# Kernel tuning notes

Measured on AMD Instinct MI355X. Metric: run time of the kernel, lower is better.

The kernel has to match this reference:

```python
import jax, jax.numpy as jnp
import numpy as np

N_NODES = 500000
D_FEAT = 128
BATCH = 16384
K_NEIGH = 32
N_MASKS = 4  # module hardcodes 4 masks with exponents 0.5*j (gcn path)


def setup_inputs() -> dict:
    key = jax.random.key(0)
    k1, k2, k3 = jax.random.split(key, 3)
    embed = jax.random.normal(k1, (N_NODES, D_FEAT), dtype=jnp.float32)
    neigh_idx = jax.random.randint(k2, (BATCH, K_NEIGH), 0, N_NODES, dtype=jnp.int32)
    # positive weights (original uses 1+degree counts; any positive weight is valid)
    neigh_w = jax.random.uniform(k3, (BATCH, K_NEIGH), dtype=jnp.float32, minval=0.05, maxval=1.0)
    return {"embed": embed, "neigh_idx": neigh_idx, "neigh_w": neigh_w}


def reference(embed, neigh_idx, neigh_w):
    # gather neighbor features: [B, K, d] (the sparse equivalent of mask.mm(embed_matrix))
    feats = embed[neigh_idx]
    # exponents 0.5*j for j = 0..3 (gcn=True branch: pow(node_weight, 0.5*j))
    exps = 0.5 * jnp.arange(N_MASKS, dtype=neigh_w.dtype)  # [4]
    W = neigh_w[None, :, :] ** exps[:, None, None]          # [4, B, K]
    # row-normalize each mask (mask.div(mask.sum(1, keepdim=True)))
    Wn = W / jnp.sum(W, axis=-1, keepdims=True)
    # weighted aggregation per mask: [4, B, d]
    out = jnp.einsum('jbk,bkd->jbd', Wn, feats)
    # concat the 4 aggregations along feature dim -> [B, 4*d]
    B = feats.shape[0]
    return jnp.moveaxis(out, 0, 1).reshape(B, N_MASKS * D_FEAT)
```

## Files before the change

kernel.cpp:

```cpp
#include <hip/hip_runtime.h>
#include <math.h>

#define BATCH 16384
#define KN 32
#define DF 128
#define NM 4
#define RPB 8

__global__ __launch_bounds__(256, 4) void wagg_kernel(
    const float* __restrict__ embed,
    const int*   __restrict__ nidx,
    const float* __restrict__ nw,
    float*       __restrict__ out)
{
    const int t  = threadIdx.x;
    const int r  = t >> 5;
    const int f  = t & 31;
    const int b  = blockIdx.x * RPB + r;

    __shared__ float4 wq[RPB][KN];
    __shared__ int    sidx[RPB][KN];
    __shared__ float4 sinv[RPB];

    {
        const float w  = nw[(size_t)b * KN + f];
        const float sq = sqrtf(w);
        float4 q;
        q.x = 1.0f; q.y = sq; q.z = w; q.w = w * sq;
        wq[r][f]   = q;
        sidx[r][f] = nidx[(size_t)b * KN + f];

        float4 s = q;
        #pragma unroll
        for (int m = 1; m < 32; m <<= 1) {
            s.x += __shfl_xor(s.x, m);
            s.y += __shfl_xor(s.y, m);
            s.z += __shfl_xor(s.z, m);
            s.w += __shfl_xor(s.w, m);
        }
        if (f == 0) {
            float4 iv;
            iv.x = 1.0f / s.x;
            iv.y = 1.0f / s.y;
            iv.z = 1.0f / s.z;
            iv.w = 1.0f / s.w;
            sinv[r] = iv;
        }
    }
    __syncthreads();

    float4 a0, a1, a2, a3;
    a0.x=a0.y=a0.z=a0.w=0.f;
    a1.x=a1.y=a1.z=a1.w=0.f;
    a2.x=a2.y=a2.z=a2.w=0.f;
    a3.x=a3.y=a3.z=a3.w=0.f;

    #pragma unroll
    for (int k = 0; k < KN; ++k) {
        const int    row = sidx[r][k];
        const float4 q   = wq[r][k];
        const float4 v   = *((const float4*)(embed + (size_t)row * DF) + f);
        a0.x += v.x;        a0.y += v.y;        a0.z += v.z;        a0.w += v.w;
        a1.x += q.y * v.x;  a1.y += q.y * v.y;  a1.z += q.y * v.z;  a1.w += q.y * v.w;
        a2.x += q.z * v.x;  a2.y += q.z * v.y;  a2.z += q.z * v.z;  a2.w += q.z * v.w;
        a3.x += q.w * v.x;  a3.y += q.w * v.y;  a3.z += q.w * v.z;  a3.w += q.w * v.w;
    }

    const float4 iv = sinv[r];
    a0.x *= iv.x; a0.y *= iv.x; a0.z *= iv.x; a0.w *= iv.x;
    a1.x *= iv.y; a1.y *= iv.y; a1.z *= iv.y; a1.w *= iv.y;
    a2.x *= iv.z; a2.y *= iv.z; a2.z *= iv.z; a2.w *= iv.z;
    a3.x *= iv.w; a3.y *= iv.w; a3.z *= iv.w; a3.w *= iv.w;

    float4* o = (float4*)(out + (size_t)b * (NM * DF));
    o[0 * 32 + f] = a0;
    o[1 * 32 + f] = a1;
    o[2 * 32 + f] = a2;
    o[3 * 32 + f] = a3;
}

extern "C" void kernel_launch(void* const* d_in, const int* in_sizes, int n_in,
                              void* d_out, int out_size, void* d_ws, size_t ws_size,
                              hipStream_t stream) {
    const float* embed = (const float*)d_in[0];
    const int*   nidx  = (const int*)  d_in[1];
    const float* nw    = (const float*)d_in[2];
    float* out = (float*)d_out;

    wagg_kernel<<<BATCH / RPB, 256, 0, stream>>>(embed, nidx, nw, out);
}
```

Before: 340.9 us.

## Split neighbor loop across wave halves with cross-half shuffle reduction

Each 64-lane wavefront now owns one batch row, and its two 32-lane halves each gather 16 of the 32 neighbors. The halves combine partial sums with a shuffle across lane offset 32, and each half then writes two of the four mask outputs. This halves the serial gather chain per thread and adds more independent memory requests per row. Rows per block drop to 4 and the occupancy hint rises to 6, at the cost of extra shuffles and fewer rows per block.

```diff
diff --git a/kernel.cpp b/kernel.cpp
--- a/kernel.cpp
+++ b/kernel.cpp
@@ -5,48 +5,43 @@
 #define KN 32
 #define DF 128
 #define NM 4
-#define RPB 8
+#define RPB 4
 
-__global__ __launch_bounds__(256, 4) void wagg_kernel(
+__global__ __launch_bounds__(256, 6) void wagg_kernel(
     const float* __restrict__ embed,
     const int*   __restrict__ nidx,
     const float* __restrict__ nw,
     float*       __restrict__ out)
 {
     const int t  = threadIdx.x;
-    const int r  = t >> 5;
-    const int f  = t & 31;
-    const int b  = blockIdx.x * RPB + r;
+    const int wv = t >> 6;
+    const int l  = t & 63;
+    const int h  = l >> 5;
+    const int f  = l & 31;
+    const int b  = blockIdx.x * RPB + wv;
 
-    __shared__ float4 wq[RPB][KN];
-    __shared__ int    sidx[RPB][KN];
-    __shared__ float4 sinv[RPB];
+    __shared__ int   sidx[RPB][KN];
+    __shared__ float sw  [RPB][KN];
+    __shared__ float ssq [RPB][KN];
 
-    {
-        const float w  = nw[(size_t)b * KN + f];
-        const float sq = sqrtf(w);
-        float4 q;
-        q.x = 1.0f; q.y = sq; q.z = w; q.w = w * sq;
-        wq[r][f]   = q;
-        sidx[r][f] = nidx[(size_t)b * KN + f];
+    const float w  = nw[(size_t)b * KN + f];
+    const float sq = sqrtf(w);
+    if (h == 0) {
+        sidx[wv][f] = nidx[(size_t)b * KN + f];
+        sw  [wv][f] = w;
+        ssq [wv][f] = sq;
+    }
 
-        float4 s = q;
-        #pragma unroll
-        for (int m = 1; m < 32; m <<= 1) {
-            s.x += __shfl_xor(s.x, m);
-            s.y += __shfl_xor(s.y, m);
-            s.z += __shfl_xor(s.z, m);
-            s.w += __shfl_xor(s.w, m);
-        }
-        if (f == 0) {
-            float4 iv;
-            iv.x = 1.0f / s.x;
-            iv.y = 1.0f / s.y;
-            iv.z = 1.0f / s.z;
-            iv.w = 1.0f / s.w;
-            sinv[r] = iv;
-        }
+    float s1 = sq;
+    float s2 = w;
+    float s3 = w * sq;
+    #pragma unroll
+    for (int m = 1; m < 32; m <<= 1) {
+        s1 += __shfl_xor(s1, m);
+        s2 += __shfl_xor(s2, m);
+        s3 += __shfl_xor(s3, m);
     }
+
     __syncthreads();
 
     float4 a0, a1, a2, a3;
@@ -55,28 +50,44 @@
     a2.x=a2.y=a2.z=a2.w=0.f;
     a3.x=a3.y=a3.z=a3.w=0.f;
 
+    const int kb = h << 4;
     #pragma unroll
-    for (int k = 0; k < KN; ++k) {
-        const int    row = sidx[r][k];
-        const float4 q   = wq[r][k];
-        const float4 v   = *((const float4*)(embed + (size_t)row * DF) + f);
+    for (int k = 0; k < 16; ++k) {
+        const int   row = sidx[wv][kb + k];
+        const float wk  = sw [wv][kb + k];
+        const float sk  = ssq[wv][kb + k];
+        const float wsk = wk * sk;
+        const float4 v  = *((const float4*)(embed + (size_t)row * DF) + f);
         a0.x += v.x;        a0.y += v.y;        a0.z += v.z;        a0.w += v.w;
-        a1.x += q.y * v.x;  a1.y += q.y * v.y;  a1.z += q.y * v.z;  a1.w += q.y * v.w;
-        a2.x += q.z * v.x;  a2.y += q.z * v.y;  a2.z += q.z * v.z;  a2.w += q.z * v.w;
-        a3.x += q.w * v.x;  a3.y += q.w * v.y;  a3.z += q.w * v.z;  a3.w += q.w * v.w;
+        a1.x += sk  * v.x;  a1.y += sk  * v.y;  a1.z += sk  * v.z;  a1.w += sk  * v.w;
+        a2.x += wk  * v.x;  a2.y += wk  * v.y;  a2.z += wk  * v.z;  a2.w += wk  * v.w;
+        a3.x += wsk * v.x;  a3.y += wsk * v.y;  a3.z += wsk * v.z;  a3.w += wsk * v.w;
     }
 
-    const float4 iv = sinv[r];
-    a0.x *= iv.x; a0.y *= iv.x; a0.z *= iv.x; a0.w *= iv.x;
-    a1.x *= iv.y; a1.y *= iv.y; a1.z *= iv.y; a1.w *= iv.y;
-    a2.x *= iv.z; a2.y *= iv.z; a2.z *= iv.z; a2.w *= iv.z;
-    a3.x *= iv.w; a3.y *= iv.w; a3.z *= iv.w; a3.w *= iv.w;
+    a0.x += __shfl_xor(a0.x, 32); a0.y += __shfl_xor(a0.y, 32);
+    a0.z += __shfl_xor(a0.z, 32); a0.w += __shfl_xor(a0.w, 32);
+    a1.x += __shfl_xor(a1.x, 32); a1.y += __shfl_xor(a1.y, 32);
+    a1.z += __shfl_xor(a1.z, 32); a1.w += __shfl_xor(a1.w, 32);
+    a2.x += __shfl_xor(a2.x, 32); a2.y += __shfl_xor(a2.y, 32);
+    a2.z += __shfl_xor(a2.z, 32); a2.w += __shfl_xor(a2.w, 32);
+    a3.x += __shfl_xor(a3.x, 32); a3.y += __shfl_xor(a3.y, 32);
+    a3.z += __shfl_xor(a3.z, 32); a3.w += __shfl_xor(a3.w, 32);
+
+    const float i0 = 1.0f / 32.0f;
+    const float i1 = 1.0f / s1;
+    const float i2 = 1.0f / s2;
+    const float i3 = 1.0f / s3;
+
+    float4 u0, u1;
+    float  c0, c1;
+    if (h == 0) { u0 = a0; c0 = i0; u1 = a1; c1 = i1; }
+    else        { u0 = a2; c0 = i2; u1 = a3; c1 = i3; }
+    u0.x *= c0; u0.y *= c0; u0.z *= c0; u0.w *= c0;
+    u1.x *= c1; u1.y *= c1; u1.z *= c1; u1.w *= c1;
 
     float4* o = (float4*)(out + (size_t)b * (NM * DF));
-    o[0 * 32 + f] = a0;
-    o[1 * 32 + f] = a1;
-    o[2 * 32 + f] = a2;
-    o[3 * 32 + f] = a3;
+    o[(2 * h)     * 32 + f] = u0;
+    o[(2 * h + 1) * 32 + f] = u1;
 }
 
 extern "C" void kernel_launch(void* const* d_in, const int* in_sizes, int n_in,
```

New measurement: 339.7 us. Within noise of the previous version (-0.4%).
